# Performance work log

Hardware: AMD Instinct MI355X
Metric: run time of the kernel (lower is better)

## Reference

```python
import jax, jax.numpy as jnp
import numpy as np

B, S, D = 8, 4096, 1024
M, K, R = 32, 3, 64
RAD = 8      # anchor_radius
KS = 3       # causal pool kernel
LN_EPS = 1e-5


def layernorm(x, g, b):
    mu = jnp.mean(x, axis=-1, keepdims=True)
    var = jnp.mean((x - mu) ** 2, axis=-1, keepdims=True)
    return (x - mu) * jax.lax.rsqrt(var + LN_EPS) * g + b


def l2norm(v, eps=1e-6):
    return v / jnp.maximum(jnp.linalg.norm(v, axis=-1, keepdims=True), eps)


def causal_pool(x, k):
    # replicate-pad front, sliding mean of width k (stride 1) via cumsum
    if k <= 1:
        return x
    xp = jnp.pad(x, ((0, 0), (k - 1, 0), (0, 0)), mode='edge')
    cs = jnp.cumsum(xp, axis=1)
    cs = jnp.pad(cs, ((0, 0), (1, 0), (0, 0)))
    return (cs[:, k:, :] - cs[:, :-k, :]) / k


def setup_inputs() -> dict:
    key = jax.random.key(0)
    ks = jax.random.split(key, 16)
    f32 = jnp.float32
    return {
        'pt_hidden': jax.random.normal(ks[0], (B, S, D), f32),
        'ts_hidden': jax.random.normal(ks[1], (B, S, D), f32),
        'patch_positions': jnp.arange(S, dtype=f32),
        'mode_centroids': jax.random.normal(ks[2], (M, D), f32),
        'stability_gate': jax.random.uniform(ks[3], (B, S, 1), f32),
        # P2TAdapter params
        'anchor_w': jax.random.normal(ks[4], (D,), f32) / np.sqrt(D),
        'anchor_b': jnp.zeros((), f32),
        'trans_a': jax.random.normal(ks[5], (M, D, R), f32) * 0.01,
        'trans_b': jax.random.normal(ks[6], (M, D, R), f32) * 0.01,
        'out_norm_g': jnp.ones((D,), f32),
        'out_norm_b': jnp.zeros((D,), f32),
        # AntiCollapseSelectiveBridge params
        'ts_norm_g': jnp.ones((D,), f32),
        'ts_norm_b': jnp.zeros((D,), f32),
        'pt_norm_g': jnp.ones((D,), f32),
        'pt_norm_b': jnp.zeros((D,), f32),
        'shared_W': jax.random.normal(ks[7], (2 * D + 1, D), f32) * 0.01,
        'shared_b': jnp.zeros((D,), f32),
        'ts_up_W': jax.random.normal(ks[8], (D, D), f32) * 0.006,
        'pt_up_W': jax.random.normal(ks[9], (D, D), f32) * 0.006,
        'bridge_scale': jnp.asarray(0.24, f32),
    }


def reference(pt_hidden, ts_hidden, patch_positions, mode_centroids, stability_gate,
              anchor_w, anchor_b, trans_a, trans_b, out_norm_g, out_norm_b,
              ts_norm_g, ts_norm_b, pt_norm_g, pt_norm_b,
              shared_W, shared_b, ts_up_W, pt_up_W, bridge_scale):
    # ---------------- P2TAdapter ----------------
    scores = jnp.einsum('bsd,d->bs', pt_hidden, anchor_w) + anchor_b        # [B,S]
    topk_scores, anchor_idx = jax.lax.top_k(scores, K)                      # [B,K]
    anchor_vectors = jnp.take_along_axis(pt_hidden, anchor_idx[..., None], axis=1)  # [B,K,D]

    basis_logits = jnp.einsum('bkd,md->bkm', l2norm(anchor_vectors), l2norm(mode_centroids))
    basis_w = jax.nn.softmax(basis_logits, axis=-1)                         # [B,K,M]
    dyn_a = jnp.einsum('bkm,mdr->bkdr', basis_w, trans_a)
    dyn_b = jnp.einsum('bkm,mdr->bkdr', basis_w, trans_b)
    low = jnp.einsum('bkd,bkdr->bkr', anchor_vectors, dyn_a)
    translated = jnp.einsum('bkr,bkdr->bkd', low, dyn_b)                    # [B,K,D]

    # neighborhood spread weights around anchors
    anchor_pos = patch_positions[anchor_idx]                                # [B,K]
    dist = jnp.abs(patch_positions[None, None, :] - anchor_pos[..., None])  # [B,K,S]
    nmask = (dist <= float(RAD)).astype(pt_hidden.dtype)
    logits = jnp.where(nmask == 0, -10000.0, -dist / float(RAD))
    spread_w = jax.nn.softmax(logits, axis=-1)                              # [B,K,S]

    anchor_update = jnp.einsum('bks,bkd->bsd', spread_w, translated)        # [B,S,D]
    ts_aug = layernorm(ts_hidden + anchor_update, out_norm_g, out_norm_b)

    # ---------------- AntiCollapseSelectiveBridge ----------------
    tsn = layernorm(ts_aug, ts_norm_g, ts_norm_b)
    ptn = layernorm(pt_hidden, pt_norm_g, pt_norm_b)
    eps = 1e-6
    dot = jnp.sum(tsn * ptn, axis=-1)
    cos = dot / (jnp.maximum(jnp.linalg.norm(tsn, axis=-1), eps) *
                 jnp.maximum(jnp.linalg.norm(ptn, axis=-1), eps))
    agreement = 0.5 * (1.0 + cos)[..., None]                                # [B,S,1]
    z = (agreement - 0.72) / 0.2
    focus = 0.2 + 0.8 * jnp.exp(-0.5 * z * z)
    bridge_gate = agreement * focus * stability_gate                        # curriculum_factor = 1

    shared = jnp.concatenate([tsn, ptn, bridge_gate], axis=-1) @ shared_W + shared_b
    shared = causal_pool(shared, KS)
    blend = jax.nn.sigmoid(bridge_scale) * 0.35
    lb = blend * bridge_gate                                                # [B,S,1]
    ts_out = ts_aug + lb * ((shared - tsn) @ ts_up_W)
    pt_out = pt_hidden + lb * ((shared - ptn) @ pt_up_W)
    return (ts_out, pt_out)
```

## Files before the change

### kernel.cpp

```cpp
#include <hip/hip_runtime.h>

#define Bn 8
#define Sn 4096
#define Dn 1024
#define Mn 32
#define Kk 3
#define Rn 64
#define BSn (Bn*Sn)
#define NBK (Bn*Kk)

typedef unsigned short u16;
typedef short short8 __attribute__((ext_vector_type(8)));
typedef float f32x4 __attribute__((ext_vector_type(4)));

__device__ __forceinline__ u16 f2bf(float f){
  unsigned u = __builtin_bit_cast(unsigned, f);
  u += 0x7fffu + ((u >> 16) & 1u);
  return (u16)(u >> 16);
}
__device__ __forceinline__ float bf2f(u16 h){
  unsigned u = ((unsigned)h) << 16;
  return __builtin_bit_cast(float, u);
}

__device__ __forceinline__ void cp16(const void* g, void* l){
  __builtin_amdgcn_global_load_lds(
      (const __attribute__((address_space(1))) void*)g,
      (__attribute__((address_space(3))) void*)l, 16, 0, 0);
}

__device__ __forceinline__ float2 block_sum2(float a, float b, float* red){
  #pragma unroll
  for (int off = 32; off > 0; off >>= 1){
    a += __shfl_down(a, off, 64);
    b += __shfl_down(b, off, 64);
  }
  int lane = threadIdx.x & 63, w = threadIdx.x >> 6;
  if (lane == 0){ red[w] = a; red[4+w] = b; }
  __syncthreads();
  float2 r;
  r.x = red[0]+red[1]+red[2]+red[3];
  r.y = red[4]+red[5]+red[6]+red[7];
  __syncthreads();
  return r;
}

__device__ __forceinline__ float3 block_sum3(float a, float b, float c, float* red){
  #pragma unroll
  for (int off = 32; off > 0; off >>= 1){
    a += __shfl_down(a, off, 64);
    b += __shfl_down(b, off, 64);
    c += __shfl_down(c, off, 64);
  }
  int lane = threadIdx.x & 63, w = threadIdx.x >> 6;
  if (lane == 0){ red[w] = a; red[4+w] = b; red[8+w] = c; }
  __syncthreads();
  float3 r;
  r.x = red[0]+red[1]+red[2]+red[3];
  r.y = red[4]+red[5]+red[6]+red[7];
  r.z = red[8]+red[9]+red[10]+red[11];
  __syncthreads();
  return r;
}

__global__ __launch_bounds__(256) void k_scores(const float* __restrict__ pt,
    const float* __restrict__ aw, const float* __restrict__ ab, float* __restrict__ scores){
  int lane = threadIdx.x & 63, w = threadIdx.x >> 6;
  int row = blockIdx.x * 4 + w;
  const float4* x  = (const float4*)(pt + (size_t)row * Dn);
  const float4* wv = (const float4*)aw;
  float acc = 0.f;
  #pragma unroll
  for (int c = 0; c < 4; c++){
    int i = c * 64 + lane;
    float4 a = x[i], b = wv[i];
    acc += a.x*b.x + a.y*b.y + a.z*b.z + a.w*b.w;
  }
  #pragma unroll
  for (int off = 32; off > 0; off >>= 1) acc += __shfl_down(acc, off, 64);
  if (lane == 0) scores[row] = acc + ab[0];
}

__global__ __launch_bounds__(256) void k_top3(const float* __restrict__ scores, int* __restrict__ aidx){
  __shared__ float tv[256*3];
  __shared__ int   ti[256*3];
  int b = blockIdx.x, t = threadIdx.x;
  float v[3] = {-1e38f, -1e38f, -1e38f};
  int  id[3] = {0x7fffffff, 0x7fffffff, 0x7fffffff};
  for (int s = t; s < Sn; s += 256){
    float sc = scores[b*Sn + s];
    if (sc > v[0] || (sc == v[0] && s < id[0])){ v[2]=v[1]; id[2]=id[1]; v[1]=v[0]; id[1]=id[0]; v[0]=sc; id[0]=s; }
    else if (sc > v[1] || (sc == v[1] && s < id[1])){ v[2]=v[1]; id[2]=id[1]; v[1]=sc; id[1]=s; }
    else if (sc > v[2] || (sc == v[2] && s < id[2])){ v[2]=sc; id[2]=s; }
  }
  for (int j = 0; j < 3; j++){ tv[t*3+j] = v[j]; ti[t*3+j] = id[j]; }
  __syncthreads();
  if (t == 0){
    float bv[3] = {-1e38f, -1e38f, -1e38f};
    int   bi[3] = {0x7fffffff, 0x7fffffff, 0x7fffffff};
    for (int c = 0; c < 256*3; c++){
      float sc = tv[c]; int ii = ti[c];
      if (sc > bv[0] || (sc == bv[0] && ii < bi[0])){ bv[2]=bv[1]; bi[2]=bi[1]; bv[1]=bv[0]; bi[1]=bi[0]; bv[0]=sc; bi[0]=ii; }
      else if (sc > bv[1] || (sc == bv[1] && ii < bi[1])){ bv[2]=bv[1]; bi[2]=bi[1]; bv[1]=sc; bi[1]=ii; }
      else if (sc > bv[2] || (sc == bv[2] && ii < bi[2])){ bv[2]=sc; bi[2]=ii; }
    }
    for (int j = 0; j < 3; j++) aidx[b*3+j] = bi[j];
  }
}

__global__ __launch_bounds__(256) void k_adapter_w(const float* __restrict__ pt,
    const float* __restrict__ cent, const float* __restrict__ pp, const int* __restrict__ aidx,
    float* __restrict__ A24, float* __restrict__ gw, float* __restrict__ invZ){
  __shared__ float a_lds[Dn];
  __shared__ float logitv[Mn];
  __shared__ float red[12];
  int bk = blockIdx.x; int b = bk / Kk;
  int t = threadIdx.x;
  int p = aidx[bk];
  const float* arow = pt + ((size_t)b*Sn + p) * Dn;
  for (int d = t; d < Dn; d += 256){ float v = arow[d]; a_lds[d] = v; A24[(size_t)bk*Dn + d] = v; }
  __syncthreads();
  float ss = 0.f;
  for (int d = t; d < Dn; d += 256){ float v = a_lds[d]; ss += v*v; }
  float2 rr0 = block_sum2(ss, 0.f, red);
  float na = fmaxf(sqrtf(rr0.x), 1e-6f);
  int lane = t & 63, w = t >> 6;
  for (int mi = 0; mi < 8; mi++){
    int m = w*8 + mi;
    const float* c = cent + (size_t)m * Dn;
    float dt = 0.f, cs = 0.f;
    for (int d = lane; d < Dn; d += 64){ float cv = c[d]; dt += a_lds[d]*cv; cs += cv*cv; }
    #pragma unroll
    for (int off = 32; off > 0; off >>= 1){ dt += __shfl_down(dt, off, 64); cs += __shfl_down(cs, off, 64); }
    if (lane == 0){ float nc = fmaxf(sqrtf(cs), 1e-6f); logitv[m] = dt / (na * nc); }
  }
  __syncthreads();
  if (t == 0){
    float mx = -1e30f;
    for (int m = 0; m < Mn; m++) mx = fmaxf(mx, logitv[m]);
    float sm = 0.f, e[Mn];
    for (int m = 0; m < Mn; m++){ e[m] = expf(logitv[m]-mx); sm += e[m]; }
    float inv = 1.f / sm;
    for (int m = 0; m < Mn; m++) gw[bk*Mn + m] = e[m] * inv;
  }
  {
    float zp = 0.f; float ppp = pp[p];
    for (int s2 = t; s2 < Sn; s2 += 256){
      float dd = fabsf(pp[s2] - ppp);
      if (dd <= 8.0f) zp += expf(-dd * 0.125f);
    }
    float2 zr = block_sum2(zp, 0.f, red);
    if (t == 0) invZ[bk] = 1.f / zr.x;
  }
}

__global__ __launch_bounds__(256) void k_lowpart(const float* __restrict__ ta,
    const float* __restrict__ A24, float* __restrict__ part_low){
  __shared__ float ta_s[64*64];
  __shared__ float a_s[NBK*64];
  int dc = blockIdx.x, m = blockIdx.y;
  int t = threadIdx.x;
  int d0 = dc * 64;
  const float4* src = (const float4*)(ta + ((size_t)m*Dn + d0) * Rn);
  float4* dst = (float4*)ta_s;
  #pragma unroll
  for (int c = 0; c < 4; c++) dst[t + c*256] = src[t + c*256];
  for (int idx = t; idx < NBK*64; idx += 256){
    int bk = idx >> 6, dl = idx & 63;
    a_s[idx] = A24[(size_t)bk*Dn + d0 + dl];
  }
  __syncthreads();
  int r = t & 63, g = t >> 6;
  #pragma unroll
  for (int j = 0; j < 6; j++){
    int bk = g*6 + j;
    float acc = 0.f;
    #pragma unroll 8
    for (int d = 0; d < 64; d++) acc += a_s[bk*64 + d] * ta_s[d*64 + r];
    part_low[(((size_t)bk*Mn + m)*16 + dc)*64 + r] = acc;
  }
}

__global__ __launch_bounds__(64) void k_lowfin(const float* __restrict__ part_low,
    const float* __restrict__ gw, float* __restrict__ lowb){
  int bk = blockIdx.x, r = threadIdx.x;
  float acc = 0.f;
  for (int m = 0; m < Mn; m++){
    float s = 0.f;
    #pragma unroll
    for (int dc = 0; dc < 16; dc++)
      s += part_low[(((size_t)bk*Mn + m)*16 + dc)*64 + r];
    acc += gw[bk*Mn + m] * s;
  }
  lowb[bk*64 + r] = acc;
}

__global__ __launch_bounds__(256) void k_transpart(const float* __restrict__ tb,
    const float* __restrict__ lowb, float* __restrict__ transp){
  __shared__ float tb_t[64*65];
  __shared__ float low_s[NBK*64];
  int dc = blockIdx.x, m = blockIdx.y;
  int t = threadIdx.x;
  int d0 = dc * 64;
  const float* src = tb + ((size_t)m*Dn + d0) * Rn;
  for (int idx = t; idx < 4096; idx += 256){
    int d = idx >> 6, r = idx & 63;
    tb_t[r*65 + d] = src[idx];
  }
  for (int idx = t; idx < NBK*64; idx += 256) low_s[idx] = lowb[idx];
  __syncthreads();
  int dl = t & 63, g = t >> 6;
  #pragma unroll
  for (int j = 0; j < 6; j++){
    int bk = g*6 + j;
    float acc = 0.f;
    #pragma unroll 8
    for (int r = 0; r < 64; r++) acc += tb_t[r*65 + dl] * low_s[bk*64 + r];
    transp[((size_t)bk*Mn + m)*Dn + d0 + dl] = acc;
  }
}

__global__ __launch_bounds__(256) void k_transfin(const float* __restrict__ transp,
    const float* __restrict__ gw, float* __restrict__ transl){
  int bk = blockIdx.x, t = threadIdx.x;
  for (int d = t; d < Dn; d += 256){
    float acc = 0.f;
    #pragma unroll 8
    for (int m = 0; m < Mn; m++)
      acc += gw[bk*Mn + m] * transp[((size_t)bk*Mn + m)*Dn + d];
    transl[(size_t)bk*Dn + d] = acc;
  }
}

__global__ __launch_bounds__(256) void k_transpose(const float* __restrict__ src,
    u16* __restrict__ dst, int Ks){
  __shared__ float tile[32][33];
  int kb = blockIdx.x * 32, nb = blockIdx.y * 32;
  int tx = threadIdx.x & 31, ty = threadIdx.x >> 5;
  #pragma unroll
  for (int r = 0; r < 32; r += 8)
    tile[ty+r][tx] = src[(size_t)(kb+ty+r) * Dn + nb + tx];
  __syncthreads();
  #pragma unroll
  for (int r = 0; r < 32; r += 8)
    dst[(size_t)(nb+ty+r) * Ks + kb + tx] = f2bf(tile[tx][ty+r]);
}

__global__ __launch_bounds__(256) void k_rows(
    const float* __restrict__ ts, const float* __restrict__ pt,
    const float* __restrict__ stab, const float* __restrict__ transl,
    const int* __restrict__ aidx, const float* __restrict__ invZ,
    const float* __restrict__ pp,
    const float* __restrict__ og, const float* __restrict__ ob,
    const float* __restrict__ tgp, const float* __restrict__ tbp,
    const float* __restrict__ pgp, const float* __restrict__ pbp,
    float* __restrict__ ts_aug_out, u16* __restrict__ Xcat, float* __restrict__ gate){
  __shared__ float red[12];
  int row = blockIdx.x; int b = row >> 12; int s = row & 4095;
  int t = threadIdx.x;
  size_t base = (size_t)row * Dn;
  const float4 xin = *(const float4*)(ts + base + 4*t);
  float x0 = xin.x, x1 = xin.y, x2 = xin.z, x3 = xin.w;
  float pps = pp[s];
  for (int k = 0; k < Kk; k++){
    int p = aidx[b*Kk + k];
    float dd = fabsf(pps - pp[p]);
    if (dd <= 8.0f){
      float coef = expf(-dd * 0.125f) * invZ[b*Kk + k];
      const float4 tr = *(const float4*)(transl + ((size_t)(b*Kk + k)) * Dn + 4*t);
      x0 += coef*tr.x; x1 += coef*tr.y; x2 += coef*tr.z; x3 += coef*tr.w;
    }
  }
  float2 r = block_sum2(x0+x1+x2+x3, x0*x0+x1*x1+x2*x2+x3*x3, red);
  float mu = r.x * (1.f/Dn); float var = r.y * (1.f/Dn) - mu*mu;
  float rs = 1.f / sqrtf(var + 1e-5f);
  float4 g4 = *(const float4*)(og + 4*t), b4 = *(const float4*)(ob + 4*t);
  float a0 = (x0-mu)*rs*g4.x + b4.x;
  float a1 = (x1-mu)*rs*g4.y + b4.y;
  float a2 = (x2-mu)*rs*g4.z + b4.z;
  float a3 = (x3-mu)*rs*g4.w + b4.w;
  float4 sto; sto.x=a0; sto.y=a1; sto.z=a2; sto.w=a3;
  *(float4*)(ts_aug_out + base + 4*t) = sto;
  r = block_sum2(a0+a1+a2+a3, a0*a0+a1*a1+a2*a2+a3*a3, red);
  mu = r.x * (1.f/Dn); var = r.y * (1.f/Dn) - mu*mu;
  rs = 1.f / sqrtf(var + 1e-5f);
  g4 = *(const float4*)(tgp + 4*t); b4 = *(const float4*)(tbp + 4*t);
  float t0 = (a0-mu)*rs*g4.x + b4.x;
  float t1 = (a1-mu)*rs*g4.y + b4.y;
  float t2 = (a2-mu)*rs*g4.z + b4.z;
  float t3 = (a3-mu)*rs*g4.w + b4.w;
  const float4 pv = *(const float4*)(pt + base + 4*t);
  r = block_sum2(pv.x+pv.y+pv.z+pv.w, pv.x*pv.x+pv.y*pv.y+pv.z*pv.z+pv.w*pv.w, red);
  mu = r.x * (1.f/Dn); var = r.y * (1.f/Dn) - mu*mu;
  rs = 1.f / sqrtf(var + 1e-5f);
  g4 = *(const float4*)(pgp + 4*t); b4 = *(const float4*)(pbp + 4*t);
  float p0 = (pv.x-mu)*rs*g4.x + b4.x;
  float p1 = (pv.y-mu)*rs*g4.y + b4.y;
  float p2 = (pv.z-mu)*rs*g4.z + b4.z;
  float p3 = (pv.w-mu)*rs*g4.w + b4.w;
  ushort4 pk;
  pk.x = f2bf(t0); pk.y = f2bf(t1); pk.z = f2bf(t2); pk.w = f2bf(t3);
  *(ushort4*)(Xcat + (size_t)row*2048 + 4*t) = pk;
  pk.x = f2bf(p0); pk.y = f2bf(p1); pk.z = f2bf(p2); pk.w = f2bf(p3);
  *(ushort4*)(Xcat + (size_t)row*2048 + Dn + 4*t) = pk;
  float3 rr = block_sum3(t0*p0+t1*p1+t2*p2+t3*p3,
                         t0*t0+t1*t1+t2*t2+t3*t3,
                         p0*p0+p1*p1+p2*p2+p3*p3, red);
  if (t == 0){
    float cosv = rr.x / (fmaxf(sqrtf(rr.y), 1e-6f) * fmaxf(sqrtf(rr.z), 1e-6f));
    float ag = 0.5f * (1.f + cosv);
    float z = (ag - 0.72f) * 5.f;
    float focus = 0.2f + 0.8f * expf(-0.5f*z*z);
    gate[row] = ag * focus * stab[row];
  }
}

__global__ __launch_bounds__(256) void k_gemm(
    const u16* __restrict__ A, const u16* __restrict__ Bt, int K, int mode,
    float* __restrict__ out0, const float* __restrict__ sbias, const float* __restrict__ Wlast,
    const float* __restrict__ gate, float* __restrict__ dts,
    const float* __restrict__ ptin, float* __restrict__ dpt, const float* __restrict__ bscale){
  __shared__ u16 As[128*32];
  __shared__ u16 Bs[128*32];
  int t = threadIdx.x; int lane = t & 63; int w = t >> 6;
  int m0 = blockIdx.x * 128, n0 = blockIdx.y * 128;
  f32x4 acc[4][4];
  #pragma unroll
  for (int i = 0; i < 4; i++)
    #pragma unroll
    for (int j = 0; j < 4; j++){ f32x4 z = {0.f,0.f,0.f,0.f}; acc[i][j] = z; }
  int qr = (w >> 1) * 64, qc = (w & 1) * 64;
  int r15 = lane & 15, quad = lane >> 4;
  int a_off[4], b_off[4];
  #pragma unroll
  for (int i = 0; i < 4; i++){
    int rr = qr + i*16 + r15;
    a_off[i] = rr*64 + ((quad ^ (rr&3)) * 16);
    int cc = qc + i*16 + r15;
    b_off[i] = cc*64 + ((quad ^ (cc&3)) * 16);
  }
  int rr0 = t >> 2;
  int gc0 = (t & 3) ^ (rr0 & 3);
  int rr1 = rr0 + 64;
  const char* ga0 = (const char*)A + ((size_t)(m0+rr0)*K)*2 + gc0*16;
  const char* ga1 = (const char*)A + ((size_t)(m0+rr1)*K)*2 + gc0*16;
  const char* gb0 = (const char*)Bt + ((size_t)(n0+rr0)*K)*2 + gc0*16;
  const char* gb1 = (const char*)Bt + ((size_t)(n0+rr1)*K)*2 + gc0*16;
  char* la0 = (char*)As + t*16; char* la1 = la0 + 4096;
  char* lb0 = (char*)Bs + t*16; char* lb1 = lb0 + 4096;
  int nk = K >> 5;
  for (int kk = 0; kk < nk; kk++){
    __syncthreads();
    cp16(ga0, la0); cp16(ga1, la1);
    cp16(gb0, lb0); cp16(gb1, lb1);
    ga0 += 64; ga1 += 64; gb0 += 64; gb1 += 64;
    __syncthreads();
    short8 af[4], bfr[4];
    #pragma unroll
    for (int i = 0; i < 4; i++) af[i]  = *(const short8*)((const char*)As + a_off[i]);
    #pragma unroll
    for (int j = 0; j < 4; j++) bfr[j] = *(const short8*)((const char*)Bs + b_off[j]);
    #pragma unroll
    for (int i = 0; i < 4; i++)
      #pragma unroll
      for (int j = 0; j < 4; j++)
        acc[i][j] = __builtin_amdgcn_mfma_f32_16x16x32_bf16(af[i], bfr[j], acc[i][j], 0, 0, 0);
  }
  float blend = 0.f;
  if (mode != 0) blend = 0.35f / (1.f + expf(-bscale[0]));
  #pragma unroll
  for (int i = 0; i < 4; i++){
    int rowb = m0 + qr + i*16 + quad*4;
    #pragma unroll
    for (int j = 0; j < 4; j++){
      int col = n0 + qc + j*16 + r15;
      #pragma unroll
      for (int rg = 0; rg < 4; rg++){
        int rw = rowb + rg;
        size_t idx = (size_t)rw * Dn + col;
        float v = acc[i][j][rg];
        if (mode == 0){
          out0[idx] = v + sbias[col] + gate[rw] * Wlast[col];
        } else if (mode == 1){
          dts[idx] = dts[idx] + blend * gate[rw] * v;
        } else {
          dpt[idx] = ptin[idx] + blend * gate[rw] * v;
        }
      }
    }
  }
}

__global__ __launch_bounds__(256) void k_pooldiff(const float* __restrict__ sh,
    const u16* __restrict__ Xcat, u16* __restrict__ Xts, u16* __restrict__ Xpt){
  int row = blockIdx.x; int s = row & 4095; int t = threadIdx.x;
  size_t base = (size_t)row * Dn + 4*t;
  int rm1 = (s >= 1) ? row-1 : row;
  int rm2 = (s >= 2) ? row-2 : rm1;
  float4 a = *(const float4*)(sh + base);
  float4 b = *(const float4*)(sh + (size_t)rm1*Dn + 4*t);
  float4 c = *(const float4*)(sh + (size_t)rm2*Dn + 4*t);
  float p0 = (a.x+b.x+c.x)*(1.f/3.f);
  float p1 = (a.y+b.y+c.y)*(1.f/3.f);
  float p2 = (a.z+b.z+c.z)*(1.f/3.f);
  float p3 = (a.w+b.w+c.w)*(1.f/3.f);
  ushort4 tn = *(const ushort4*)(Xcat + (size_t)row*2048 + 4*t);
  ushort4 pn = *(const ushort4*)(Xcat + (size_t)row*2048 + Dn + 4*t);
  ushort4 o;
  o.x = f2bf(p0 - bf2f(tn.x)); o.y = f2bf(p1 - bf2f(tn.y));
  o.z = f2bf(p2 - bf2f(tn.z)); o.w = f2bf(p3 - bf2f(tn.w));
  *(ushort4*)(Xts + base) = o;
  o.x = f2bf(p0 - bf2f(pn.x)); o.y = f2bf(p1 - bf2f(pn.y));
  o.z = f2bf(p2 - bf2f(pn.z)); o.w = f2bf(p3 - bf2f(pn.w));
  *(ushort4*)(Xpt + base) = o;
}

extern "C" void kernel_launch(void* const* d_in, const int* in_sizes, int n_in,
                              void* d_out, int out_size, void* d_ws, size_t ws_size,
                              hipStream_t stream){
  const float* pt   = (const float*)d_in[0];
  const float* ts   = (const float*)d_in[1];
  const float* pp   = (const float*)d_in[2];
  const float* cent = (const float*)d_in[3];
  const float* stab = (const float*)d_in[4];
  const float* aw   = (const float*)d_in[5];
  const float* ab   = (const float*)d_in[6];
  const float* ta   = (const float*)d_in[7];
  const float* tb   = (const float*)d_in[8];
  const float* og   = (const float*)d_in[9];
  const float* ob   = (const float*)d_in[10];
  const float* tg   = (const float*)d_in[11];
  const float* tbn  = (const float*)d_in[12];
  const float* pg   = (const float*)d_in[13];
  const float* pb   = (const float*)d_in[14];
  const float* sW   = (const float*)d_in[15];
  const float* sb   = (const float*)d_in[16];
  const float* tsW  = (const float*)d_in[17];
  const float* ptW  = (const float*)d_in[18];
  const float* bsc  = (const float*)d_in[19];
  float* out_ts = (float*)d_out;
  float* out_pt = out_ts + (size_t)BSn * Dn;

  char* wbase = (char*)d_ws; size_t off = 0;
  auto alloc = [&](size_t bytes) -> void* {
    void* p = wbase + off;
    off += (bytes + 255) & ~(size_t)255;
    return p;
  };
  float* scores  = (float*)alloc((size_t)BSn * 4);
  int*   aidx    = (int*)  alloc(256);
  float* invZ    = (float*)alloc(256);
  float* transl  = (float*)alloc((size_t)NBK*Dn * 4);
  float* gate    = (float*)alloc((size_t)BSn * 4);
  float* A24     = (float*)alloc((size_t)NBK*Dn * 4);
  float* gw      = (float*)alloc((size_t)NBK*Mn * 4);
  float* part_low= (float*)alloc((size_t)NBK*Mn*16*64 * 4);
  float* lowb    = (float*)alloc((size_t)NBK*64 * 4);
  float* transp  = (float*)alloc((size_t)NBK*Mn*Dn * 4);
  u16*   Xcat    = (u16*)  alloc((size_t)BSn * 2048 * 2);
  float* shmem   = (float*)alloc((size_t)BSn * Dn * 4);
  u16*   Xts     = (u16*)  alloc((size_t)BSn * Dn * 2);
  u16*   Xpt     = (u16*)  alloc((size_t)BSn * Dn * 2);
  u16*   WtS     = (u16*)  alloc((size_t)Dn * 2048 * 2);
  u16*   WtT     = (u16*)  alloc((size_t)Dn * Dn * 2);
  u16*   WtP     = (u16*)  alloc((size_t)Dn * Dn * 2);

  k_scores<<<BSn/4, 256, 0, stream>>>(pt, aw, ab, scores);
  k_top3<<<Bn, 256, 0, stream>>>(scores, aidx);
  k_adapter_w<<<NBK, 256, 0, stream>>>(pt, cent, pp, aidx, A24, gw, invZ);
  k_lowpart<<<dim3(16, Mn), 256, 0, stream>>>(ta, A24, part_low);
  k_lowfin<<<NBK, 64, 0, stream>>>(part_low, gw, lowb);
  k_transpart<<<dim3(16, Mn), 256, 0, stream>>>(tb, lowb, transp);
  k_transfin<<<NBK, 256, 0, stream>>>(transp, gw, transl);
  k_transpose<<<dim3(64,32), 256, 0, stream>>>(sW, WtS, 2048);
  k_transpose<<<dim3(32,32), 256, 0, stream>>>(tsW, WtT, 1024);
  k_transpose<<<dim3(32,32), 256, 0, stream>>>(ptW, WtP, 1024);
  k_rows<<<BSn, 256, 0, stream>>>(ts, pt, stab, transl, aidx, invZ, pp,
                                  og, ob, tg, tbn, pg, pb, out_ts, Xcat, gate);
  k_gemm<<<dim3(BSn/128, Dn/128), 256, 0, stream>>>(Xcat, WtS, 2048, 0,
      shmem, sb, sW + (size_t)2048*Dn, gate, nullptr, nullptr, nullptr, bsc);
  k_pooldiff<<<BSn, 256, 0, stream>>>(shmem, Xcat, Xts, Xpt);
  k_gemm<<<dim3(BSn/128, Dn/128), 256, 0, stream>>>(Xts, WtT, 1024, 1,
      nullptr, nullptr, nullptr, gate, out_ts, nullptr, nullptr, bsc);
  k_gemm<<<dim3(BSn/128, Dn/128), 256, 0, stream>>>(Xpt, WtP, 1024, 2,
      nullptr, nullptr, nullptr, gate, nullptr, pt, out_pt, bsc);
}
```

Before: 1.553 ms.

## Rewrite GEMM as 256x256 tile, 8-wave, double-buffered pipelined MFMA kernel

Replaces the 128x128, 4-wave, single-buffered GEMM with a 256x256 block tile, 8 waves, a K-step of 64 and double-buffered LDS (128KB). Global-to-LDS copies for upcoming tiles are interleaved with four MFMA quadrant phases, using explicit barriers, waitcnt and setprio. Block IDs are remapped for L2 locality. The aim is to hide memory latency and raise data reuse per block, at the cost of heavy LDS and register use and fragile hand-tuned synchronisation.

```diff
diff --git a/kernel.cpp b/kernel.cpp
--- a/kernel.cpp
+++ b/kernel.cpp
@@ -315,70 +315,135 @@
   }
 }
 
-__global__ __launch_bounds__(256) void k_gemm(
+__global__ __launch_bounds__(512, 2) void k_gemm(
     const u16* __restrict__ A, const u16* __restrict__ Bt, int K, int mode,
     float* __restrict__ out0, const float* __restrict__ sbias, const float* __restrict__ Wlast,
     const float* __restrict__ gate, float* __restrict__ dts,
     const float* __restrict__ ptin, float* __restrict__ dpt, const float* __restrict__ bscale){
-  __shared__ u16 As[128*32];
-  __shared__ u16 Bs[128*32];
-  int t = threadIdx.x; int lane = t & 63; int w = t >> 6;
-  int m0 = blockIdx.x * 128, n0 = blockIdx.y * 128;
-  f32x4 acc[4][4];
-  #pragma unroll
-  for (int i = 0; i < 4; i++)
+  __shared__ __attribute__((aligned(16))) char smem[131072];
+  const int NT = K >> 6;
+  const int tid = threadIdx.x;
+  const int lane = tid & 63, w = tid >> 6;
+  const int wm = w >> 2, wn = w & 3;
+  const int r15 = lane & 15, quad = lane >> 4;
+  const int bid = blockIdx.x;
+  const int bm = (bid & 7) * 16 + ((bid >> 3) & 15);
+  const int bn = bid >> 7;
+  const int m0 = bm * 256, n0 = bn * 256;
+
+  const int row0 = tid >> 3, j0 = tid & 7;
+  const int js = j0 ^ (row0 & 7);
+  const size_t rowbytes = (size_t)K * 2;
+  const char* gA = (const char*)A + (size_t)(m0 + row0) * rowbytes + js * 16;
+  const char* gB = (const char*)Bt + (size_t)(n0 + row0) * rowbytes + js * 16;
+  const size_t rstep64 = rowbytes << 6;
+  char* lA = smem + tid * 16;
+  char* lB = smem + 65536 + tid * 16;
+
+  auto stgA = [&](int half, int tile, int buf){
+    const char* s = gA + (size_t)half * (rstep64 << 1) + (size_t)tile * 128;
+    char* d = lA + buf * 32768 + half * 16384;
+    cp16(s, d); cp16(s + rstep64, d + 8192);
+  };
+  auto stgB = [&](int half, int tile, int buf){
+    const char* s = gB + (size_t)half * (rstep64 << 1) + (size_t)tile * 128;
+    char* d = lB + buf * 32768 + half * 16384;
+    cp16(s, d); cp16(s + rstep64, d + 8192);
+  };
+
+  int aoff[4][2], boff[2][2];
+  #pragma unroll
+  for (int fi = 0; fi < 4; fi++){
+    int rl = wm*64 + fi*16 + r15;
+    #pragma unroll
+    for (int ks = 0; ks < 2; ks++)
+      aoff[fi][ks] = rl*128 + ((((ks<<2) + quad) ^ (r15 & 7)) << 4);
+  }
+  #pragma unroll
+  for (int fj = 0; fj < 2; fj++){
+    int rn = wn*32 + fj*16 + r15;
+    #pragma unroll
+    for (int ks = 0; ks < 2; ks++)
+      boff[fj][ks] = rn*128 + ((((ks<<2) + quad) ^ (r15 & 7)) << 4);
+  }
+
+  short8 ar[4][2];
+  short8 br[2][2][2];
+  f32x4 acc[8][4];
+  #pragma unroll
+  for (int i = 0; i < 8; i++)
     #pragma unroll
     for (int j = 0; j < 4; j++){ f32x4 z = {0.f,0.f,0.f,0.f}; acc[i][j] = z; }
-  int qr = (w >> 1) * 64, qc = (w & 1) * 64;
-  int r15 = lane & 15, quad = lane >> 4;
-  int a_off[4], b_off[4];
-  #pragma unroll
-  for (int i = 0; i < 4; i++){
-    int rr = qr + i*16 + r15;
-    a_off[i] = rr*64 + ((quad ^ (rr&3)) * 16);
-    int cc = qc + i*16 + r15;
-    b_off[i] = cc*64 + ((quad ^ (cc&3)) * 16);
-  }
-  int rr0 = t >> 2;
-  int gc0 = (t & 3) ^ (rr0 & 3);
-  int rr1 = rr0 + 64;
-  const char* ga0 = (const char*)A + ((size_t)(m0+rr0)*K)*2 + gc0*16;
-  const char* ga1 = (const char*)A + ((size_t)(m0+rr1)*K)*2 + gc0*16;
-  const char* gb0 = (const char*)Bt + ((size_t)(n0+rr0)*K)*2 + gc0*16;
-  const char* gb1 = (const char*)Bt + ((size_t)(n0+rr1)*K)*2 + gc0*16;
-  char* la0 = (char*)As + t*16; char* la1 = la0 + 4096;
-  char* lb0 = (char*)Bs + t*16; char* lb1 = lb0 + 4096;
-  int nk = K >> 5;
-  for (int kk = 0; kk < nk; kk++){
-    __syncthreads();
-    cp16(ga0, la0); cp16(ga1, la1);
-    cp16(gb0, lb0); cp16(gb1, lb1);
-    ga0 += 64; ga1 += 64; gb0 += 64; gb1 += 64;
-    __syncthreads();
-    short8 af[4], bfr[4];
-    #pragma unroll
-    for (int i = 0; i < 4; i++) af[i]  = *(const short8*)((const char*)As + a_off[i]);
-    #pragma unroll
-    for (int j = 0; j < 4; j++) bfr[j] = *(const short8*)((const char*)Bs + b_off[j]);
-    #pragma unroll
-    for (int i = 0; i < 4; i++)
+
+  auto rdA = [&](int ph, int buf){
+    #pragma unroll
+    for (int fi = 0; fi < 4; fi++)
       #pragma unroll
-      for (int j = 0; j < 4; j++)
-        acc[i][j] = __builtin_amdgcn_mfma_f32_16x16x32_bf16(af[i], bfr[j], acc[i][j], 0, 0, 0);
-  }
+      for (int ks = 0; ks < 2; ks++)
+        ar[fi][ks] = *(const short8*)(smem + buf*32768 + ph*16384 + aoff[fi][ks]);
+  };
+  auto rdB = [&](int p, int buf){
+    #pragma unroll
+    for (int fj = 0; fj < 2; fj++)
+      #pragma unroll
+      for (int ks = 0; ks < 2; ks++)
+        br[p][fj][ks] = *(const short8*)(smem + 65536 + buf*32768 + p*16384 + boff[fj][ks]);
+  };
+  auto mma16 = [&](int ap, int bp){
+    __builtin_amdgcn_s_barrier();
+    asm volatile("s_waitcnt lgkmcnt(0)" ::: "memory");
+    __builtin_amdgcn_sched_barrier(0);
+    __builtin_amdgcn_s_setprio(1);
+    #pragma unroll
+    for (int fi = 0; fi < 4; fi++)
+      #pragma unroll
+      for (int fj = 0; fj < 2; fj++)
+        #pragma unroll
+        for (int ks = 0; ks < 2; ks++)
+          acc[ap*4+fi][bp*2+fj] = __builtin_amdgcn_mfma_f32_16x16x32_bf16(
+              ar[fi][ks], br[bp][fj][ks], acc[ap*4+fi][bp*2+fj], 0, 0, 0);
+    __builtin_amdgcn_s_setprio(0);
+  };
+
+  stgA(0, 0, 0); stgA(1, 0, 0); stgB(0, 0, 0); stgB(1, 0, 0);
+  stgA(0, 1, 1); stgB(1, 1, 1);
+  asm volatile("s_waitcnt vmcnt(4)" ::: "memory");
+  __builtin_amdgcn_s_barrier();
+
+  auto tileStep = [&](int t, int buf){
+    rdA(0, buf); rdB(0, buf);
+    if (t+1 < NT) stgA(1, t+1, buf^1);
+    mma16(0, 0);
+    __builtin_amdgcn_s_barrier();
+    rdB(1, buf);
+    if (t+1 < NT) stgB(0, t+1, buf^1);
+    mma16(0, 1);
+    __builtin_amdgcn_s_barrier();
+    rdA(1, buf);
+    if (t+2 < NT) stgA(0, t+2, buf);
+    mma16(1, 1);
+    __builtin_amdgcn_s_barrier();
+    if (t+2 < NT) stgB(1, t+2, buf);
+    mma16(1, 0);
+    if (t+2 < NT){ asm volatile("s_waitcnt vmcnt(4)" ::: "memory"); }
+    else         { asm volatile("s_waitcnt vmcnt(0)" ::: "memory"); }
+    __builtin_amdgcn_s_barrier();
+  };
+  for (int t = 0; t < NT; t += 2){ tileStep(t, 0); tileStep(t+1, 1); }
+
   float blend = 0.f;
   if (mode != 0) blend = 0.35f / (1.f + expf(-bscale[0]));
   #pragma unroll
-  for (int i = 0; i < 4; i++){
-    int rowb = m0 + qr + i*16 + quad*4;
-    #pragma unroll
-    for (int j = 0; j < 4; j++){
-      int col = n0 + qc + j*16 + r15;
+  for (int mi = 0; mi < 8; mi++){
+    int rowb = m0 + (mi>>2)*128 + wm*64 + (mi&3)*16 + quad*4;
+    #pragma unroll
+    for (int nj = 0; nj < 4; nj++){
+      int col = n0 + (nj>>1)*128 + wn*32 + (nj&1)*16 + r15;
       #pragma unroll
       for (int rg = 0; rg < 4; rg++){
         int rw = rowb + rg;
         size_t idx = (size_t)rw * Dn + col;
-        float v = acc[i][j][rg];
+        float v = acc[mi][nj][rg];
         if (mode == 0){
           out0[idx] = v + sbias[col] + gate[rw] * Wlast[col];
         } else if (mode == 1){
@@ -477,11 +542,11 @@
   k_transpose<<<dim3(32,32), 256, 0, stream>>>(ptW, WtP, 1024);
   k_rows<<<BSn, 256, 0, stream>>>(ts, pt, stab, transl, aidx, invZ, pp,
                                   og, ob, tg, tbn, pg, pb, out_ts, Xcat, gate);
-  k_gemm<<<dim3(BSn/128, Dn/128), 256, 0, stream>>>(Xcat, WtS, 2048, 0,
+  k_gemm<<<512, 512, 0, stream>>>(Xcat, WtS, 2048, 0,
       shmem, sb, sW + (size_t)2048*Dn, gate, nullptr, nullptr, nullptr, bsc);
   k_pooldiff<<<BSn, 256, 0, stream>>>(shmem, Xcat, Xts, Xpt);
-  k_gemm<<<dim3(BSn/128, Dn/128), 256, 0, stream>>>(Xts, WtT, 1024, 1,
+  k_gemm<<<512, 512, 0, stream>>>(Xts, WtT, 1024, 1,
       nullptr, nullptr, nullptr, gate, out_ts, nullptr, nullptr, bsc);
-  k_gemm<<<dim3(BSn/128, Dn/128), 256, 0, stream>>>(Xpt, WtP, 1024, 2,
+  k_gemm<<<512, 512, 0, stream>>>(Xpt, WtP, 1024, 2,
       nullptr, nullptr, nullptr, gate, nullptr, pt, out_pt, bsc);
 }
```

New measurement: 1.444 ms. -7.1%, faster.
